# Kernel optimization log

Measured on AMD Instinct MI355X. Metric: run time of the kernel, lower is better.

## Reference

```python
import jax, jax.numpy as jnp
import numpy as np

B, T, C, HEAD = 8, 2048, 1024, 64

def setup_inputs() -> dict:
    key = jax.random.key(0)
    kx, kq, kk, kv = jax.random.split(key, 4)
    bound = 1.0 / np.sqrt(C)  # torch Linear default init range
    x = jax.random.normal(kx, (B, T, C), dtype=jnp.float32)
    Wq = jax.random.uniform(kq, (C, HEAD), jnp.float32, -bound, bound)
    Wk = jax.random.uniform(kk, (C, HEAD), jnp.float32, -bound, bound)
    Wv = jax.random.uniform(kv, (C, HEAD), jnp.float32, -bound, bound)
    return {"x": x, "Wq": Wq, "Wk": Wk, "Wv": Wv}

def reference(x, Wq, Wk, Wv):
    Bn, Tn, Cn = x.shape
    q = jnp.einsum('btc,ch->bth', x, Wq)  # [B,T,H]
    k = jnp.einsum('btc,ch->bth', x, Wk)
    v = jnp.einsum('btc,ch->bth', x, Wv)
    # NOTE: original scales by C**-0.5 (input channels), not head_size**-0.5
    scale = Cn ** (-0.5)
    w = jnp.einsum('bqh,bkh->bqk', q, k) * scale  # [B,T,T]
    causal = jnp.tril(jnp.ones((Tn, Tn), dtype=bool))
    w = jnp.where(causal, w, -jnp.inf)
    wei = jax.nn.softmax(w, axis=-1)
    return jnp.einsum('bqk,bkh->bqh', wei, v)  # [B,T,H]
```

## Files before the change

kernel.cpp:

```cpp
#include <hip/hip_runtime.h>
#include <hip/hip_bf16.h>

#define B_ 8
#define T_ 2048
#define C_ 1024
#define H_ 64

typedef __bf16 bf16x8 __attribute__((ext_vector_type(8)));
typedef float f32x4 __attribute__((ext_vector_type(4)));

typedef __attribute__((address_space(3))) unsigned int lds_u32;
typedef const __attribute__((address_space(1))) unsigned int glb_u32;
__device__ __forceinline__ void gl_lds16(const void* gp, void* lp) {
  __builtin_amdgcn_global_load_lds((glb_u32*)gp, (lds_u32*)lp, 16, 0, 0);
}

__global__ __launch_bounds__(256) void prep_w_k(const float* __restrict__ Wq,
                                                const float* __restrict__ Wk,
                                                const float* __restrict__ Wv,
                                                __bf16* __restrict__ Wt) {
  int idx = blockIdx.x * 256 + threadIdx.x;
  int m = idx >> 14;
  int rem = idx & 16383;
  int h = rem >> 8;
  int c4 = (rem & 255) << 2;
  const float* W = (m == 0) ? Wq : ((m == 1) ? Wk : Wv);
  float sc = (m == 0) ? 0.03125f : 1.0f;
  __bf16* dst = Wt + ((size_t)(m * H_ + h)) * C_ + c4;
#pragma unroll
  for (int i = 0; i < 4; ++i) dst[i] = (__bf16)(W[(size_t)(c4 + i) * H_ + h] * sc);
}

__global__ __launch_bounds__(256) void qkv_k(const float* __restrict__ x,
                                             const __bf16* __restrict__ Wt,
                                             __bf16* __restrict__ q,
                                             __bf16* __restrict__ kk,
                                             __bf16* __restrict__ vt) {
  __shared__ __align__(16) char smem[65536];
  const int tid = threadIdx.x;
  const int lane = tid & 63;
  const int wc = tid >> 6;
  const int l15 = lane & 15;
  const int g = lane >> 4;
  const int row0 = blockIdx.x * 32;

  const int srow = tid >> 3;
  const int sch = (tid & 7) ^ (srow & 7);
  const char* agsrc = (const char*)(x + (size_t)(row0 + srow) * C_) + sch * 16;
  const int adst = tid * 16;
  const char* bgs[3];
#pragma unroll
  for (int i = 0; i < 3; ++i) {
    int c = i * 256 + tid;
    int bg = c / 192;
    int bcol = c - bg * 192;
    bgs[i] = (const char*)Wt + bcol * 2048 + bg * 16;
  }
  const int bdst = 4096 + tid * 16;

  f32x4 acc[2][3];
#pragma unroll
  for (int rt = 0; rt < 2; ++rt)
#pragma unroll
    for (int ctl = 0; ctl < 3; ++ctl) acc[rt][ctl] = (f32x4)0.0f;

  auto stage = [&](int t, int bufo) {
    const size_t ao = (size_t)t << 7;
    const size_t bo = (size_t)t << 6;
    gl_lds16(agsrc + ao, smem + bufo + adst);
    gl_lds16(bgs[0] + bo, smem + bufo + bdst);
    gl_lds16(bgs[1] + bo, smem + bufo + 4096 + bdst);
    gl_lds16(bgs[2] + bo, smem + bufo + 8192 + bdst);
  };

  stage(0, 0);
  stage(1, 16384);
  stage(2, 32768);

  for (int t = 0; t < 32; ++t) {
    const int rem = 31 - t;
    if (rem >= 2) {
      asm volatile("s_waitcnt vmcnt(8)" ::: "memory");
    } else if (rem == 1) {
      asm volatile("s_waitcnt vmcnt(4)" ::: "memory");
    } else {
      asm volatile("s_waitcnt vmcnt(0)" ::: "memory");
    }
    __builtin_amdgcn_s_barrier();
    if (t + 3 < 32) stage(t + 3, ((t + 3) & 3) << 14);
    const int cur = (t & 3) << 14;
    bf16x8 af[2];
#pragma unroll
    for (int rt = 0; rt < 2; ++rt) {
      const int row = rt * 16 + l15;
      const char* ab = smem + cur + row * 128;
      f32x4 a0 = *(const f32x4*)(ab + ((((g << 1)) ^ (row & 7)) << 4));
      f32x4 a1 = *(const f32x4*)(ab + ((((g << 1) | 1) ^ (row & 7)) << 4));
#pragma unroll
      for (int j = 0; j < 4; ++j) {
        af[rt][j] = (__bf16)a0[j];
        af[rt][4 + j] = (__bf16)a1[j];
      }
    }
#pragma unroll
    for (int ctl = 0; ctl < 3; ++ctl) {
      const int col = wc * 48 + ctl * 16 + l15;
      bf16x8 bf = *(const bf16x8*)(smem + cur + 4096 + g * 3072 + col * 16);
      acc[0][ctl] = __builtin_amdgcn_mfma_f32_16x16x32_bf16(af[0], bf, acc[0][ctl], 0, 0, 0);
      acc[1][ctl] = __builtin_amdgcn_mfma_f32_16x16x32_bf16(af[1], bf, acc[1][ctl], 0, 0, 0);
    }
  }

#pragma unroll
  for (int rt = 0; rt < 2; ++rt)
#pragma unroll
    for (int ctl = 0; ctl < 3; ++ctl) {
      const int cb = wc * 48 + ctl * 16;
      const int m = cb >> 6;
      const int drow = row0 + rt * 16 + g * 4;
      if (m == 0) {
#pragma unroll
        for (int r = 0; r < 4; ++r)
          q[(size_t)(drow + r) * H_ + (cb & 63) + l15] = (__bf16)acc[rt][ctl][r];
      } else if (m == 1) {
#pragma unroll
        for (int r = 0; r < 4; ++r)
          kk[(size_t)(drow + r) * H_ + (cb & 63) + l15] = (__bf16)acc[rt][ctl][r];
      } else {
        const int vh = (cb - 128) + l15;
        const int t0 = rt * 16 + g * 4;
        union { ushort4 u; __bf16 h[4]; } pk;
#pragma unroll
        for (int r = 0; r < 4; ++r) pk.h[r] = (__bf16)acc[rt][ctl][r];
        int off = ((vh * 32 + t0) * 2) ^ ((vh & 7) << 4);
        *(ushort4*)(smem + off) = pk.u;
      }
    }
  __syncthreads();
  {
    const int h = tid >> 2;
    const int t8 = (tid & 3) * 8;
    const int sw = (h & 7) << 4;
    unsigned long long u0 = *(const unsigned long long*)(smem + (((h * 32 + t8) * 2) ^ sw));
    unsigned long long u1 = *(const unsigned long long*)(smem + (((h * 32 + t8 + 4) * 2) ^ sw));
    const int bb = blockIdx.x >> 6;
    const int tglob = (blockIdx.x & 63) * 32 + t8;
    unsigned long long* dst =
        (unsigned long long*)(vt + ((size_t)bb * 64 + h) * T_ + tglob);
    dst[0] = u0;
    dst[1] = u1;
  }
}

template <int SPLIT>
__global__ __launch_bounds__(256) void attn_k(const __bf16* __restrict__ q,
                                              const __bf16* __restrict__ k,
                                              const __bf16* __restrict__ vt,
                                              float* __restrict__ Opart,
                                              float2* __restrict__ ml) {
  __shared__ __align__(16) char smem[57344];
  const int bid = blockIdx.x;
  const int p = bid % SPLIT;
  const int qb = (bid / SPLIT) & 31;
  const int b = bid / (SPLIT * 32);
  const int tid = threadIdx.x;
  const int lane = tid & 63;
  const int w = tid >> 6;
  const int l15 = lane & 15;
  const int g = lane >> 4;
  const size_t qkbase = (size_t)b * T_ * H_;
  const int qr0 = qb * 64 + w * 16;

  const __bf16* qp = q + qkbase + (size_t)(qr0 + l15) * H_ + g * 8;
  bf16x8 aq0 = *(const bf16x8*)qp;
  bf16x8 aq1 = *(const bf16x8*)(qp + 32);

  const int r0c = tid >> 3, x0c = (tid & 7) ^ (r0c & 7);
  const int r1c = (tid + 256) >> 3, x1c = (tid & 7) ^ (r1c & 7);
  const __bf16* ks0 = k + qkbase + (size_t)r0c * H_ + x0c * 8;
  const __bf16* ks1 = k + qkbase + (size_t)r1c * H_ + x1c * 8;
  const __bf16* vbase = vt + (size_t)b * 64 * T_;
  const __bf16* vs0 = vbase + (size_t)r0c * T_ + x0c * 8;
  const __bf16* vs1 = vbase + (size_t)r1c * T_ + x1c * 8;
  const int d0 = tid * 16, d1 = 4096 + tid * 16;

  auto stage = [&](int kvb, int bufo) {
    gl_lds16(ks0 + (size_t)kvb * H_, smem + bufo + d0);
    gl_lds16(ks1 + (size_t)kvb * H_, smem + bufo + d1);
    gl_lds16(vs0 + kvb, smem + bufo + 8192 + d0);
    gl_lds16(vs1 + kvb, smem + bufo + 8192 + d1);
  };

  f32x4 accO[4];
#pragma unroll
  for (int i = 0; i < 4; ++i) accO[i] = (f32x4)0.0f;
  float mrow[4] = {-1e30f, -1e30f, -1e30f, -1e30f};
  float lsum[4] = {0.f, 0.f, 0.f, 0.f};
  char* pb = smem + 49152 + w * 2048;

  const int len = (qb + SPLIT) / SPLIT;
  const int kb0 = p * len;
  int kbend = kb0 + len;
  if (kbend > qb + 1) kbend = qb + 1;
  const int n = kbend - kb0;

  if (n > 0) {
    stage(kb0 * 64, 0);
    if (n > 1) stage((kb0 + 1) * 64, 16384);
    for (int i = 0; i < n; ++i) {
      if (i + 1 < n) {
        asm volatile("s_waitcnt vmcnt(4)" ::: "memory");
      } else {
        asm volatile("s_waitcnt vmcnt(0)" ::: "memory");
      }
      __builtin_amdgcn_s_barrier();
      if (i + 2 < n) stage((kb0 + i + 2) * 64, ((i + 2) % 3) * 16384);
      const int kb = kb0 + i;
      const int kvb = kb * 64;
      const char* kbuf = smem + (i % 3) * 16384;
      const char* vbuf = kbuf + 8192;
      f32x4 s[4];
#pragma unroll
      for (int ct = 0; ct < 4; ++ct) {
        const int row = ct * 16 + l15;
        bf16x8 b0 = *(const bf16x8*)(kbuf + row * 128 + ((g ^ (row & 7)) << 4));
        bf16x8 b1 = *(const bf16x8*)(kbuf + row * 128 + (((g + 4) ^ (row & 7)) << 4));
        f32x4 z = (f32x4)0.0f;
        z = __builtin_amdgcn_mfma_f32_16x16x32_bf16(aq0, b0, z, 0, 0, 0);
        z = __builtin_amdgcn_mfma_f32_16x16x32_bf16(aq1, b1, z, 0, 0, 0);
        s[ct] = z;
      }
      if (kb == qb) {
#pragma unroll
        for (int ct = 0; ct < 4; ++ct)
#pragma unroll
          for (int r = 0; r < 4; ++r)
            if (kvb + ct * 16 + l15 > qr0 + g * 4 + r) s[ct][r] = -1e30f;
      }
      float al[4];
#pragma unroll
      for (int r = 0; r < 4; ++r) {
        float v = fmaxf(fmaxf(s[0][r], s[1][r]), fmaxf(s[2][r], s[3][r]));
        v = fmaxf(v, __shfl_xor(v, 1, 64));
        v = fmaxf(v, __shfl_xor(v, 2, 64));
        v = fmaxf(v, __shfl_xor(v, 4, 64));
        v = fmaxf(v, __shfl_xor(v, 8, 64));
        float m2 = fmaxf(mrow[r], v);
        al[r] = __expf(mrow[r] - m2);
        mrow[r] = m2;
      }
#pragma unroll
      for (int ct = 0; ct < 4; ++ct)
#pragma unroll
        for (int r = 0; r < 4; ++r) s[ct][r] = __expf(s[ct][r] - mrow[r]);
#pragma unroll
      for (int r = 0; r < 4; ++r) {
        lsum[r] = lsum[r] * al[r] + (s[0][r] + s[1][r]) + (s[2][r] + s[3][r]);
#pragma unroll
        for (int hct = 0; hct < 4; ++hct) accO[hct][r] *= al[r];
      }
#pragma unroll
      for (int ct = 0; ct < 4; ++ct)
#pragma unroll
        for (int r = 0; r < 4; ++r) {
          int qrow = g * 4 + r;
          int off = ((qrow * 64 + ct * 16 + l15) * 2) ^ ((qrow & 7) << 4);
          *(__bf16*)(pb + off) = (__bf16)s[ct][r];
        }
#pragma unroll
      for (int ks = 0; ks < 2; ++ks) {
        int off = ((l15 * 64 + ks * 32 + g * 8) * 2) ^ ((l15 & 7) << 4);
        bf16x8 pa = *(const bf16x8*)(pb + off);
#pragma unroll
        for (int hct = 0; hct < 4; ++hct) {
          const int h = hct * 16 + l15;
          const int chunk = ks * 4 + g;
          bf16x8 bv = *(const bf16x8*)(vbuf + h * 128 + ((chunk ^ (h & 7)) << 4));
          accO[hct] = __builtin_amdgcn_mfma_f32_16x16x32_bf16(pa, bv, accO[hct], 0, 0, 0);
        }
      }
    }
  }
#pragma unroll
  for (int r = 0; r < 4; ++r) {
    float v = lsum[r];
    v += __shfl_xor(v, 1, 64);
    v += __shfl_xor(v, 2, 64);
    v += __shfl_xor(v, 4, 64);
    v += __shfl_xor(v, 8, 64);
    lsum[r] = v;
  }
  float* op = Opart + ((size_t)p * (B_ * T_) + (size_t)b * T_ + qr0) * H_;
#pragma unroll
  for (int hct = 0; hct < 4; ++hct)
#pragma unroll
    for (int r = 0; r < 4; ++r)
      op[(size_t)(g * 4 + r) * H_ + hct * 16 + l15] = accO[hct][r];
  if (l15 == 0) {
#pragma unroll
    for (int r = 0; r < 4; ++r)
      ml[(size_t)p * (B_ * T_) + (size_t)b * T_ + qr0 + g * 4 + r] =
          make_float2(mrow[r], lsum[r]);
  }
}

template <int SPLIT>
__global__ __launch_bounds__(256) void comb_k(const float* __restrict__ Opart,
                                              const float2* __restrict__ ml,
                                              float* __restrict__ out) {
  int gid = blockIdx.x * 256 + threadIdx.x;
  int row = gid >> 4;
  int h4 = (gid & 15) * 4;
  float m[SPLIT], l[SPLIT];
#pragma unroll
  for (int p = 0; p < SPLIT; ++p) {
    float2 t = ml[(size_t)p * (B_ * T_) + row];
    m[p] = t.x;
    l[p] = t.y;
  }
  float M = -1e30f;
#pragma unroll
  for (int p = 0; p < SPLIT; ++p) M = fmaxf(M, m[p]);
  float wp[SPLIT], wsum = 0.f;
#pragma unroll
  for (int p = 0; p < SPLIT; ++p) {
    wp[p] = __expf(m[p] - M);
    wsum += wp[p] * l[p];
  }
  float4 o = make_float4(0.f, 0.f, 0.f, 0.f);
#pragma unroll
  for (int p = 0; p < SPLIT; ++p) {
    float4 a = *(const float4*)(Opart + ((size_t)p * (B_ * T_) + row) * H_ + h4);
    o.x += wp[p] * a.x;
    o.y += wp[p] * a.y;
    o.z += wp[p] * a.z;
    o.w += wp[p] * a.w;
  }
  float inv = 1.0f / wsum;
  *(float4*)(out + (size_t)row * H_ + h4) =
      make_float4(o.x * inv, o.y * inv, o.z * inv, o.w * inv);
}

extern "C" void kernel_launch(void* const* d_in, const int* in_sizes, int n_in,
                              void* d_out, int out_size, void* d_ws, size_t ws_size,
                              hipStream_t stream) {
  const float* x  = (const float*)d_in[0];
  const float* Wq = (const float*)d_in[1];
  const float* Wk = (const float*)d_in[2];
  const float* Wv = (const float*)d_in[3];
  float* out = (float*)d_out;
  char* ws = (char*)d_ws;
  __bf16* Wt   = (__bf16*)ws;
  __bf16* qb   = (__bf16*)(ws + 0x60000);
  __bf16* kb   = (__bf16*)(ws + 0x260000);
  __bf16* vtb  = (__bf16*)(ws + 0x460000);
  float*  Op   = (float*)(ws + 0x660000);
  float2* mlb  = (float2*)(ws + 0xE60000);

  hipLaunchKernelGGL(prep_w_k, dim3(192), dim3(256), 0, stream, Wq, Wk, Wv, Wt);
  hipLaunchKernelGGL(qkv_k, dim3(512), dim3(256), 0, stream, x, Wt, qb, kb, vtb);
  hipLaunchKernelGGL(attn_k<2>, dim3(8 * 32 * 2), dim3(256), 0, stream, qb, kb, vtb, Op, mlb);
  hipLaunchKernelGGL(comb_k<2>, dim3(1024), dim3(256), 0, stream, Op, mlb, out);
}
```

Measured before the change: 165.2 us.

## Deepen attention K/V prefetch to four buffers and pre-tile QKV weights

The attention kernel's K/V pipeline moves from three LDS buffers to four, prefetching three blocks ahead with adjusted vmcnt waits. This hides more global-load latency at the cost of 72KB LDS per block, which may reduce occupancy. The weight prep kernel now writes bf16 weights in a tiled layout so that each qkv_k stage loads B tiles from contiguous addresses. This replaces the strided per-thread gathers and their division arithmetic.

```diff
diff --git a/kernel.cpp b/kernel.cpp
--- a/kernel.cpp
+++ b/kernel.cpp
@@ -18,21 +18,25 @@
 __global__ __launch_bounds__(256) void prep_w_k(const float* __restrict__ Wq,
                                                 const float* __restrict__ Wk,
                                                 const float* __restrict__ Wv,
-                                                __bf16* __restrict__ Wt) {
+                                                __bf16* __restrict__ Wt2) {
   int idx = blockIdx.x * 256 + threadIdx.x;
   int m = idx >> 14;
   int rem = idx & 16383;
   int h = rem >> 8;
-  int c4 = (rem & 255) << 2;
+  int cb = (rem & 255) * 4;
   const float* W = (m == 0) ? Wq : ((m == 1) ? Wk : Wv);
   float sc = (m == 0) ? 0.03125f : 1.0f;
-  __bf16* dst = Wt + ((size_t)(m * H_ + h)) * C_ + c4;
-#pragma unroll
-  for (int i = 0; i < 4; ++i) dst[i] = (__bf16)(W[(size_t)(c4 + i) * H_ + h] * sc);
+  const int col = m * 64 + h;
+  const int t = cb >> 5;
+  const int g = (cb >> 3) & 3;
+  const int j = cb & 7;
+  __bf16* dst = Wt2 + (((size_t)(t * 4 + g) * 192 + col) * 8 + j);
+#pragma unroll
+  for (int i = 0; i < 4; ++i) dst[i] = (__bf16)(W[(size_t)(cb + i) * H_ + h] * sc);
 }
 
 __global__ __launch_bounds__(256) void qkv_k(const float* __restrict__ x,
-                                             const __bf16* __restrict__ Wt,
+                                             const __bf16* __restrict__ Wt2,
                                              __bf16* __restrict__ q,
                                              __bf16* __restrict__ kk,
                                              __bf16* __restrict__ vt) {
@@ -48,15 +52,7 @@
   const int sch = (tid & 7) ^ (srow & 7);
   const char* agsrc = (const char*)(x + (size_t)(row0 + srow) * C_) + sch * 16;
   const int adst = tid * 16;
-  const char* bgs[3];
-#pragma unroll
-  for (int i = 0; i < 3; ++i) {
-    int c = i * 256 + tid;
-    int bg = c / 192;
-    int bcol = c - bg * 192;
-    bgs[i] = (const char*)Wt + bcol * 2048 + bg * 16;
-  }
-  const int bdst = 4096 + tid * 16;
+  const char* b2src = (const char*)Wt2 + tid * 16;
 
   f32x4 acc[2][3];
 #pragma unroll
@@ -65,12 +61,11 @@
     for (int ctl = 0; ctl < 3; ++ctl) acc[rt][ctl] = (f32x4)0.0f;
 
   auto stage = [&](int t, int bufo) {
-    const size_t ao = (size_t)t << 7;
-    const size_t bo = (size_t)t << 6;
-    gl_lds16(agsrc + ao, smem + bufo + adst);
-    gl_lds16(bgs[0] + bo, smem + bufo + bdst);
-    gl_lds16(bgs[1] + bo, smem + bufo + 4096 + bdst);
-    gl_lds16(bgs[2] + bo, smem + bufo + 8192 + bdst);
+    gl_lds16(agsrc + ((size_t)t << 7), smem + bufo + adst);
+    const char* bs = b2src + (size_t)t * 12288;
+    gl_lds16(bs, smem + bufo + 4096 + tid * 16);
+    gl_lds16(bs + 4096, smem + bufo + 8192 + tid * 16);
+    gl_lds16(bs + 8192, smem + bufo + 12288 + tid * 16);
   };
 
   stage(0, 0);
@@ -158,7 +153,7 @@
                                               const __bf16* __restrict__ vt,
                                               float* __restrict__ Opart,
                                               float2* __restrict__ ml) {
-  __shared__ __align__(16) char smem[57344];
+  __shared__ __align__(16) char smem[73728];
   const int bid = blockIdx.x;
   const int p = bid % SPLIT;
   const int qb = (bid / SPLIT) & 31;
@@ -174,6 +169,7 @@
   const __bf16* qp = q + qkbase + (size_t)(qr0 + l15) * H_ + g * 8;
   bf16x8 aq0 = *(const bf16x8*)qp;
   bf16x8 aq1 = *(const bf16x8*)(qp + 32);
+  asm volatile("s_waitcnt vmcnt(0)" ::: "memory");
 
   const int r0c = tid >> 3, x0c = (tid & 7) ^ (r0c & 7);
   const int r1c = (tid + 256) >> 3, x1c = (tid & 7) ^ (r1c & 7);
@@ -196,7 +192,7 @@
   for (int i = 0; i < 4; ++i) accO[i] = (f32x4)0.0f;
   float mrow[4] = {-1e30f, -1e30f, -1e30f, -1e30f};
   float lsum[4] = {0.f, 0.f, 0.f, 0.f};
-  char* pb = smem + 49152 + w * 2048;
+  char* pb = smem + 65536 + w * 2048;
 
   const int len = (qb + SPLIT) / SPLIT;
   const int kb0 = p * len;
@@ -207,17 +203,21 @@
   if (n > 0) {
     stage(kb0 * 64, 0);
     if (n > 1) stage((kb0 + 1) * 64, 16384);
+    if (n > 2) stage((kb0 + 2) * 64, 32768);
     for (int i = 0; i < n; ++i) {
-      if (i + 1 < n) {
+      const int remn = n - 1 - i;
+      if (remn >= 2) {
+        asm volatile("s_waitcnt vmcnt(8)" ::: "memory");
+      } else if (remn == 1) {
         asm volatile("s_waitcnt vmcnt(4)" ::: "memory");
       } else {
         asm volatile("s_waitcnt vmcnt(0)" ::: "memory");
       }
       __builtin_amdgcn_s_barrier();
-      if (i + 2 < n) stage((kb0 + i + 2) * 64, ((i + 2) % 3) * 16384);
+      if (i + 3 < n) stage((kb0 + i + 3) * 64, ((i + 3) & 3) << 14);
       const int kb = kb0 + i;
       const int kvb = kb * 64;
-      const char* kbuf = smem + (i % 3) * 16384;
+      const char* kbuf = smem + ((i & 3) << 14);
       const char* vbuf = kbuf + 8192;
       f32x4 s[4];
 #pragma unroll
@@ -350,15 +350,15 @@
   const float* Wv = (const float*)d_in[3];
   float* out = (float*)d_out;
   char* ws = (char*)d_ws;
-  __bf16* Wt   = (__bf16*)ws;
+  __bf16* Wt2  = (__bf16*)ws;
   __bf16* qb   = (__bf16*)(ws + 0x60000);
   __bf16* kb   = (__bf16*)(ws + 0x260000);
   __bf16* vtb  = (__bf16*)(ws + 0x460000);
   float*  Op   = (float*)(ws + 0x660000);
   float2* mlb  = (float2*)(ws + 0xE60000);
 
-  hipLaunchKernelGGL(prep_w_k, dim3(192), dim3(256), 0, stream, Wq, Wk, Wv, Wt);
-  hipLaunchKernelGGL(qkv_k, dim3(512), dim3(256), 0, stream, x, Wt, qb, kb, vtb);
+  hipLaunchKernelGGL(prep_w_k, dim3(192), dim3(256), 0, stream, Wq, Wk, Wv, Wt2);
+  hipLaunchKernelGGL(qkv_k, dim3(512), dim3(256), 0, stream, x, Wt2, qb, kb, vtb);
   hipLaunchKernelGGL(attn_k<2>, dim3(8 * 32 * 2), dim3(256), 0, stream, qb, kb, vtb, Op, mlb);
   hipLaunchKernelGGL(comb_k<2>, dim3(1024), dim3(256), 0, stream, Op, mlb, out);
 }
```

Result: faster. 147.8 us (-10.5%).
